# Kernel optimization log

Measured on AMD Instinct MI355X. Metric: run time of the kernel, lower is better.

## Reference

```python
import jax, jax.numpy as jnp
import numpy as np

EPS_LN = 1e-5
MASK_BIAS = -1e9


def setup_inputs() -> dict:
    key = jax.random.key(0)
    ks = jax.random.split(key, 8)
    B, S, R, C = 1, 512, 64, 8   # batch, N_seq, N_res, channels
    H, CH = 8, 1                 # n_head, c_h
    m = jax.random.normal(ks[0], (B, S, R, C), dtype=jnp.float32)
    msa_mask = jax.random.randint(ks[1], (B, S, R), 0, 2).astype(jnp.float32)
    # learned parameters
    ln_w = jnp.ones((C,), jnp.float32)
    ln_b = jnp.zeros((C,), jnp.float32)
    sc = 1.0 / np.sqrt(C)
    wq = jax.random.normal(ks[2], (H * CH, C), jnp.float32) * sc
    wk = jax.random.normal(ks[3], (CH, C), jnp.float32) * sc
    wv = jax.random.normal(ks[4], (CH, C), jnp.float32) * sc
    wg = jax.random.normal(ks[5], (H * CH, C), jnp.float32) * sc
    bg = jnp.zeros((H * CH,), jnp.float32)
    wo = jax.random.normal(ks[6], (C, H * CH), jnp.float32) * (1.0 / np.sqrt(H * CH))
    bo = jnp.zeros((C,), jnp.float32)
    return {"m": m, "msa_mask": msa_mask, "ln_w": ln_w, "ln_b": ln_b,
            "wq": wq, "wk": wk, "wv": wv, "wg": wg, "bg": bg,
            "wo": wo, "bo": bo}


def reference(m, msa_mask, ln_w, ln_b, wq, wk, wv, wg, bg, wo, bo):
    H, CH = 8, 1
    # transpose so attention runs over the sequence axis per residue column
    mt = jnp.swapaxes(m, 1, 2)            # [B, i, s, c]
    mask = jnp.swapaxes(msa_mask, 1, 2)   # [B, i, s]
    B, I, S, C = mt.shape
    # layernorm over channels
    mu = jnp.mean(mt, axis=-1, keepdims=True)
    var = jnp.mean(jnp.square(mt - mu), axis=-1, keepdims=True)
    m_norm = (mt - mu) / jnp.sqrt(var + EPS_LN) * ln_w + ln_b
    # masked mean-pooled global query
    denom = jnp.sum(mask, axis=-1, keepdims=True) + 1e-5       # [B, i, 1]
    q_global = jnp.sum(m_norm * mask[..., None], axis=-2) / denom  # [B, i, c]
    q = (q_global @ wq.T).reshape(B, I, H, CH)                 # [B, i, h, c_h]
    k = m_norm @ wk.T                                          # [B, i, s, c_h]
    v = m_norm @ wv.T                                          # [B, i, s, c_h]
    gate = jax.nn.sigmoid(m_norm @ wg.T + bg).reshape(B, I, S, H, CH)
    # broadcast global query over s, zero masked query positions
    q_rep = q[:, :, :, None, :] * mask[:, :, None, :, None]    # [B, i, h, s, c_h]
    scale = 1.0 / jnp.sqrt(jnp.asarray(CH, mt.dtype))
    scores = jnp.einsum('bihqd,bikd->bihqk', q_rep, k) * scale  # [B, i, h, s, s]
    pair_mask = (mask[:, :, None, :, None] * mask[:, :, None, None, :]) > 0
    scores = jnp.where(pair_mask, scores, MASK_BIAS)
    attn = jax.nn.softmax(scores, axis=-1)
    o = jnp.einsum('bihqk,bikd->bihqd', attn, v)               # [B, i, h, s, c_h]
    o = jnp.transpose(o, (0, 1, 3, 2, 4))                      # [B, i, s, h, c_h]
    o = o * gate * mask[:, :, :, None, None]
    o = o.reshape(B, I, S, H * CH) @ wo.T + bo                 # [B, i, s, c]
    return jnp.swapaxes(o, 1, 2)                               # [B, s, i, c]
```

## Files before the change

kernel.cpp:

```cpp
#include <hip/hip_runtime.h>
#include <math.h>

#define S_SEQ 512
#define R_RES 64
#define C_CH  8
#define H_HD  8

__global__ __launch_bounds__(512) void msa_col_global_attn(
    const float* __restrict__ m,
    const float* __restrict__ mask_g,
    const float* __restrict__ ln_w,
    const float* __restrict__ ln_b,
    const float* __restrict__ wq,
    const float* __restrict__ wk,
    const float* __restrict__ wv,
    const float* __restrict__ wg,
    const float* __restrict__ bg,
    const float* __restrict__ wo,
    const float* __restrict__ bo,
    float* __restrict__ out)
{
    const int i    = blockIdx.x;
    const int s    = threadIdx.x;
    const int wave = s >> 6;
    const int lane = s & 63;

    __shared__ float sred[8][17];

    const float* mp = m + (s * R_RES + i) * C_CH;
    float4 a0 = *(const float4*)(mp);
    float4 a1 = *(const float4*)(mp + 4);
    float x[8] = {a0.x, a0.y, a0.z, a0.w, a1.x, a1.y, a1.z, a1.w};
    const float msk   = mask_g[s * R_RES + i];
    const bool  valid = (msk > 0.f);

    float mu = 0.f;
    #pragma unroll
    for (int c = 0; c < 8; ++c) mu += x[c];
    mu *= 0.125f;
    float var = 0.f;
    #pragma unroll
    for (int c = 0; c < 8; ++c) { float d = x[c] - mu; var += d * d; }
    var *= 0.125f;
    const float rinv = rsqrtf(var + 1e-5f);
    float n[8];
    #pragma unroll
    for (int c = 0; c < 8; ++c) n[c] = (x[c] - mu) * rinv * ln_w[c] + ln_b[c];

    float kv = 0.f, vv = 0.f;
    #pragma unroll
    for (int c = 0; c < 8; ++c) { kv += n[c] * wk[c]; vv += n[c] * wv[c]; }

    float r[11];
    #pragma unroll
    for (int c = 0; c < 8; ++c) r[c] = n[c] * msk;
    r[8]  = msk;
    r[9]  = valid ? kv : -INFINITY;
    r[10] = valid ? kv :  INFINITY;
    #pragma unroll
    for (int d = 1; d < 64; d <<= 1) {
        #pragma unroll
        for (int j = 0; j < 9; ++j) r[j] += __shfl_xor(r[j], d, 64);
        r[9]  = fmaxf(r[9],  __shfl_xor(r[9],  d, 64));
        r[10] = fminf(r[10], __shfl_xor(r[10], d, 64));
    }
    if (lane == 0) {
        #pragma unroll
        for (int j = 0; j < 11; ++j) sred[wave][j] = r[j];
    }
    __syncthreads();

    float qg[8] = {0,0,0,0,0,0,0,0};
    float cnt = 0.f, kmax = -INFINITY, kmin = INFINITY;
    #pragma unroll
    for (int w = 0; w < 8; ++w) {
        #pragma unroll
        for (int c = 0; c < 8; ++c) qg[c] += sred[w][c];
        cnt  += sred[w][8];
        kmax = fmaxf(kmax, sred[w][9]);
        kmin = fminf(kmin, sred[w][10]);
    }
    const float rdenom = 1.f / (cnt + 1e-5f);
    float qgn[8];
    #pragma unroll
    for (int c = 0; c < 8; ++c) qgn[c] = qg[c] * rdenom;

    float qh[8];
    #pragma unroll
    for (int h = 0; h < 8; ++h) {
        float acc = 0.f;
        #pragma unroll
        for (int c = 0; c < 8; ++c) acc += qgn[c] * wq[h * 8 + c];
        qh[h] = acc;
    }

    float r2[16];
    #pragma unroll
    for (int h = 0; h < 8; ++h) {
        const float rowmax = (qh[h] >= 0.f) ? qh[h] * kmax : qh[h] * kmin;
        const float e = valid ? __expf(qh[h] * kv - rowmax) : 0.f;
        r2[h]     = e;
        r2[8 + h] = e * vv;
    }
    #pragma unroll
    for (int d = 1; d < 64; d <<= 1) {
        #pragma unroll
        for (int j = 0; j < 16; ++j) r2[j] += __shfl_xor(r2[j], d, 64);
    }
    __syncthreads();
    if (lane == 0) {
        #pragma unroll
        for (int j = 0; j < 16; ++j) sred[wave][j] = r2[j];
    }
    __syncthreads();

    float ctx[8];
    #pragma unroll
    for (int h = 0; h < 8; ++h) {
        float Z = 0.f, Cs = 0.f;
        #pragma unroll
        for (int w = 0; w < 8; ++w) { Z += sred[w][h]; Cs += sred[w][8 + h]; }
        ctx[h] = (Z > 0.f) ? (Cs / Z) : 0.f;
    }

    float o8[8];
    #pragma unroll
    for (int c = 0; c < 8; ++c) o8[c] = bo[c];
    if (valid) {
        #pragma unroll
        for (int h = 0; h < 8; ++h) {
            float g = bg[h];
            #pragma unroll
            for (int c = 0; c < 8; ++c) g += n[c] * wg[h * 8 + c];
            const float gate = 1.f / (1.f + __expf(-g));
            const float oh = gate * ctx[h];
            #pragma unroll
            for (int c = 0; c < 8; ++c) o8[c] += oh * wo[c * 8 + h];
        }
    }
    float* op = out + (s * R_RES + i) * C_CH;
    *(float4*)(op)     = make_float4(o8[0], o8[1], o8[2], o8[3]);
    *(float4*)(op + 4) = make_float4(o8[4], o8[5], o8[6], o8[7]);
}

extern "C" void kernel_launch(void* const* d_in, const int* in_sizes, int n_in,
                              void* d_out, int out_size, void* d_ws, size_t ws_size,
                              hipStream_t stream) {
    const float* m     = (const float*)d_in[0];
    const float* mmask = (const float*)d_in[1];
    const float* ln_w  = (const float*)d_in[2];
    const float* ln_b  = (const float*)d_in[3];
    const float* wq    = (const float*)d_in[4];
    const float* wk    = (const float*)d_in[5];
    const float* wv    = (const float*)d_in[6];
    const float* wg    = (const float*)d_in[7];
    const float* bg    = (const float*)d_in[8];
    const float* wo    = (const float*)d_in[9];
    const float* bo    = (const float*)d_in[10];
    float* out = (float*)d_out;

    msa_col_global_attn<<<dim3(R_RES), dim3(S_SEQ), 0, stream>>>(
        m, mmask, ln_w, ln_b, wq, wk, wv, wg, bg, wo, bo, out);
}
```

Measured before the change: 84.51 us.

## Stage k/v/mask in LDS and assign one head per wave for softmax sums

Each thread writes its k, v and mask values to shared memory, and each wave then computes the softmax numerator and denominator for a single head across all 512 sequence positions. This replaces the 16-value cross-lane shuffle reduction over the whole block with two values per wave. It removes one barrier and vectorises the partial-sum reads, and the gate projection is moved earlier so it can overlap the reduction. In exchange it uses more LDS and holds more registers across the barrier.

```diff
diff --git a/kernel.cpp b/kernel.cpp
--- a/kernel.cpp
+++ b/kernel.cpp
@@ -25,7 +25,11 @@
     const int wave = s >> 6;
     const int lane = s & 63;
 
-    __shared__ float sred[8][17];
+    __shared__ __align__(16) float kvs[S_SEQ];
+    __shared__ __align__(16) float vvs[S_SEQ];
+    __shared__ __align__(16) float mks[S_SEQ];
+    __shared__ __align__(16) float part[8][12];
+    __shared__ __align__(16) float ctxs[8];
 
     const float* mp = m + (s * R_RES + i) * C_CH;
     float4 a0 = *(const float4*)(mp);
@@ -51,6 +55,19 @@
     #pragma unroll
     for (int c = 0; c < 8; ++c) { kv += n[c] * wk[c]; vv += n[c] * wv[c]; }
 
+    float gh[8];
+    #pragma unroll
+    for (int h = 0; h < 8; ++h) {
+        float g = bg[h];
+        #pragma unroll
+        for (int c = 0; c < 8; ++c) g += n[c] * wg[h * 8 + c];
+        gh[h] = g;
+    }
+
+    kvs[s] = kv;
+    vvs[s] = vv;
+    mks[s] = msk;
+
     float r[11];
     #pragma unroll
     for (int c = 0; c < 8; ++c) r[c] = n[c] * msk;
@@ -66,7 +83,7 @@
     }
     if (lane == 0) {
         #pragma unroll
-        for (int j = 0; j < 11; ++j) sred[wave][j] = r[j];
+        for (int j = 0; j < 11; ++j) part[wave][j] = r[j];
     }
     __syncthreads();
 
@@ -74,54 +91,54 @@
     float cnt = 0.f, kmax = -INFINITY, kmin = INFINITY;
     #pragma unroll
     for (int w = 0; w < 8; ++w) {
-        #pragma unroll
-        for (int c = 0; c < 8; ++c) qg[c] += sred[w][c];
-        cnt  += sred[w][8];
-        kmax = fmaxf(kmax, sred[w][9]);
-        kmin = fminf(kmin, sred[w][10]);
+        float4 p0 = *(const float4*)&part[w][0];
+        float4 p1 = *(const float4*)&part[w][4];
+        float4 p2 = *(const float4*)&part[w][8];
+        qg[0] += p0.x; qg[1] += p0.y; qg[2] += p0.z; qg[3] += p0.w;
+        qg[4] += p1.x; qg[5] += p1.y; qg[6] += p1.z; qg[7] += p1.w;
+        cnt += p2.x;
+        kmax = fmaxf(kmax, p2.y);
+        kmin = fminf(kmin, p2.z);
     }
     const float rdenom = 1.f / (cnt + 1e-5f);
-    float qgn[8];
-    #pragma unroll
-    for (int c = 0; c < 8; ++c) qgn[c] = qg[c] * rdenom;
-
     float qh[8];
     #pragma unroll
     for (int h = 0; h < 8; ++h) {
         float acc = 0.f;
         #pragma unroll
-        for (int c = 0; c < 8; ++c) acc += qgn[c] * wq[h * 8 + c];
+        for (int c = 0; c < 8; ++c) acc += (qg[c] * rdenom) * wq[h * 8 + c];
         qh[h] = acc;
     }
 
-    float r2[16];
-    #pragma unroll
-    for (int h = 0; h < 8; ++h) {
-        const float rowmax = (qh[h] >= 0.f) ? qh[h] * kmax : qh[h] * kmin;
-        const float e = valid ? __expf(qh[h] * kv - rowmax) : 0.f;
-        r2[h]     = e;
-        r2[8 + h] = e * vv;
-    }
-    #pragma unroll
-    for (int d = 1; d < 64; d <<= 1) {
+    {
+        const float q = qh[wave];
+        const float rowmax = (q >= 0.f) ? q * kmax : q * kmin;
+        const int base = lane * 8;
+        float4 k0 = *(const float4*)&kvs[base], k1 = *(const float4*)&kvs[base + 4];
+        float4 v0 = *(const float4*)&vvs[base], v1 = *(const float4*)&vvs[base + 4];
+        float4 m0 = *(const float4*)&mks[base], m1 = *(const float4*)&mks[base + 4];
+        float kk[8] = {k0.x,k0.y,k0.z,k0.w,k1.x,k1.y,k1.z,k1.w};
+        float vk[8] = {v0.x,v0.y,v0.z,v0.w,v1.x,v1.y,v1.z,v1.w};
+        float mk[8] = {m0.x,m0.y,m0.z,m0.w,m1.x,m1.y,m1.z,m1.w};
+        float sz = 0.f, sc = 0.f;
         #pragma unroll
-        for (int j = 0; j < 16; ++j) r2[j] += __shfl_xor(r2[j], d, 64);
-    }
-    __syncthreads();
-    if (lane == 0) {
+        for (int j = 0; j < 8; ++j) {
+            const float e = (mk[j] > 0.f) ? __expf(q * kk[j] - rowmax) : 0.f;
+            sz += e;
+            sc += e * vk[j];
+        }
         #pragma unroll
-        for (int j = 0; j < 16; ++j) sred[wave][j] = r2[j];
+        for (int d = 1; d < 64; d <<= 1) {
+            sz += __shfl_xor(sz, d, 64);
+            sc += __shfl_xor(sc, d, 64);
+        }
+        if (lane == 0) ctxs[wave] = (sz > 0.f) ? (sc / sz) : 0.f;
     }
     __syncthreads();
 
-    float ctx[8];
-    #pragma unroll
-    for (int h = 0; h < 8; ++h) {
-        float Z = 0.f, Cs = 0.f;
-        #pragma unroll
-        for (int w = 0; w < 8; ++w) { Z += sred[w][h]; Cs += sred[w][8 + h]; }
-        ctx[h] = (Z > 0.f) ? (Cs / Z) : 0.f;
-    }
+    float4 c0 = *(const float4*)&ctxs[0];
+    float4 c1 = *(const float4*)&ctxs[4];
+    float ctx[8] = {c0.x,c0.y,c0.z,c0.w,c1.x,c1.y,c1.z,c1.w};
 
     float o8[8];
     #pragma unroll
@@ -129,10 +146,7 @@
     if (valid) {
         #pragma unroll
         for (int h = 0; h < 8; ++h) {
-            float g = bg[h];
-            #pragma unroll
-            for (int c = 0; c < 8; ++c) g += n[c] * wg[h * 8 + c];
-            const float gate = 1.f / (1.f + __expf(-g));
+            const float gate = 1.f / (1.f + __expf(-gh[h]));
             const float oh = gate * ctx[h];
             #pragma unroll
             for (int c = 0; c < 8; ++c) o8[c] += oh * wo[c * 8 + h];
```

After: 79.32 us. 1.07x faster.
